# Optimization experiments

Hardware: AMD Instinct MI355X
Metric: run time of the kernel (lower is better)

Reference implementation:

```python
import jax, jax.numpy as jnp
import numpy as np

B, S, H, I, E, K = 2, 512, 512, 1024, 64, 4


def setup_inputs() -> dict:
    key = jax.random.key(0)
    ks = jax.random.split(key, 16)
    scale = jnp.float32(0.02)

    def w(k, shape):
        return jax.random.normal(k, shape, dtype=jnp.float32) * scale

    return {
        "x": jax.random.normal(ks[0], (B, S, H), dtype=jnp.float32),
        "router_w": w(ks[1], (E, H)),
        "router_b": w(ks[2], (E,)),
        "expert_biases": jnp.zeros((E,), dtype=jnp.float32),
        "sw1": w(ks[3], (I, H)), "sb1": w(ks[4], (I,)),
        "sw2": w(ks[5], (H, I)), "sb2": w(ks[6], (H,)),
        "sw3": w(ks[7], (I, H)), "sb3": w(ks[8], (I,)),
        "w1": w(ks[9], (E, I, H)), "b1": w(ks[10], (E, I)),
        "w2": w(ks[11], (E, H, I)), "b2": w(ks[12], (E, H)),
        "w3": w(ks[13], (E, I, H)), "b3": w(ks[14], (E, I)),
        "top_k": K,
    }


def _ffn(x, w1, b1, w2, b2, w3, b3):
    return (jax.nn.silu(x @ w1.T + b1) * (x @ w3.T + b3)) @ w2.T + b2


def reference(x, router_w, router_b, expert_biases,
              sw1, sb1, sw2, sb2, sw3, sb3,
              w1, b1, w2, b2, w3, b3, top_k):
    Bx, Sx, Hx = x.shape
    Ex = router_w.shape[0]

    # Router: logits [B,S,E]; top-k selection uses bias-adjusted logits,
    # but gates come from the ORIGINAL (unbiased) logits.
    logits = x @ router_w.T + router_b
    _, idx = jax.lax.top_k(logits + expert_biases, top_k)  # [B,S,K] int32
    orig = jnp.take_along_axis(logits, idx, axis=-1)       # [B,S,K]
    scores = jax.nn.sigmoid(orig)
    gates = scores / jnp.maximum(jnp.sum(scores, axis=-1, keepdims=True), 1e-12)

    # Shared expert(s): num_shared_experts == 1, divided by 1.
    shared = _ffn(x, sw1, sb1, sw2, sb2, sw3, sb3)

    # Combine gates into a dense per-token per-expert gate matrix [T,E].
    xf = x.reshape(-1, Hx)                 # [T,H]
    T = xf.shape[0]
    tok = jnp.arange(T)[:, None]
    gate_full = jnp.zeros((T, Ex), x.dtype).at[tok, idx.reshape(T, top_k)].add(
        gates.reshape(T, top_k))

    # Routed experts: each expert FFN over all tokens, gated combine.
    # (Mathematically identical to the original masked-dense loop: the mask
    #  zeroes both inputs and gates of unassigned tokens.)
    def body(acc, p):
        ew1, eb1, ew2, eb2, ew3, eb3, g = p
        y = _ffn(xf, ew1, eb1, ew2, eb2, ew3, eb3)  # [T,H]
        return acc + g[:, None] * y, None

    acc, _ = jax.lax.scan(body, jnp.zeros_like(xf),
                          (w1, b1, w2, b2, w3, b3, gate_full.T))

    return shared + acc.reshape(x.shape)
```

## Files before the change

### kernel.cpp

```cpp
#include <hip/hip_runtime.h>
#include <math.h>

#define T_    1024
#define H_    512
#define I_    1024
#define E_    64
#define K_    4
#define NPAIR (T_*K_)
#define NENT  (NPAIR + T_)

#define BM 64
#define BN 64
#define BKS 64
#define LDP 72
#define MAXWORK 160

typedef float  f32x4  __attribute__((ext_vector_type(4)));
typedef short  bf16x8 __attribute__((ext_vector_type(8)));

__device__ __forceinline__ ushort f2bf(float f) {
    uint u = __float_as_uint(f);
    u += 0x7fffu + ((u >> 16) & 1u);
    return (ushort)(u >> 16);
}

__global__ __launch_bounds__(64) void moe_router(
    const float* __restrict__ x, const float* __restrict__ rw,
    const float* __restrict__ rb, const float* __restrict__ eb,
    int* __restrict__ idx_out, float* __restrict__ gate_out)
{
    const int t = blockIdx.x;
    const int lane = threadIdx.x;
    __shared__ float xs[H_];
    __shared__ float lg[E_];
    __shared__ float bs[E_];
    for (int i = lane; i < H_; i += 64) xs[i] = x[(size_t)t*H_ + i];
    bs[lane] = eb[lane];
    __syncthreads();
    float acc = 0.f;
    const float* wrow = rw + (size_t)lane*H_;
    for (int k = 0; k < H_; k += 4) {
        float4 w4 = *reinterpret_cast<const float4*>(wrow + k);
        acc = fmaf(xs[k+0], w4.x, acc);
        acc = fmaf(xs[k+1], w4.y, acc);
        acc = fmaf(xs[k+2], w4.z, acc);
        acc = fmaf(xs[k+3], w4.w, acc);
    }
    lg[lane] = acc + rb[lane];
    __syncthreads();
    if (lane == 0) {
        unsigned long long used = 0ull;
        int sel[K_]; float orig[K_];
        for (int k = 0; k < K_; ++k) {
            float best = -INFINITY; int bi = 0;
            for (int e = 0; e < E_; ++e) {
                if (used & (1ull << e)) continue;
                float v = lg[e] + bs[e];
                if (v > best) { best = v; bi = e; }
            }
            used |= (1ull << bi);
            sel[k] = bi; orig[k] = lg[bi];
        }
        float s[K_]; float sum = 0.f;
        for (int k = 0; k < K_; ++k) { s[k] = 1.f/(1.f + __expf(-orig[k])); sum += s[k]; }
        sum = fmaxf(sum, 1e-12f);
        for (int k = 0; k < K_; ++k) {
            idx_out[t*K_ + k] = sel[k];
            gate_out[t*K_ + k] = s[k] / sum;
        }
    }
}

__global__ __launch_bounds__(256) void moe_build(
    const int* __restrict__ idx, const float* __restrict__ gates,
    int* __restrict__ cnts, int* __restrict__ offs,
    int* __restrict__ entry_token, float* __restrict__ entry_gate,
    int* __restrict__ pair_pos,
    int* __restrict__ blk_e, int* __restrict__ blk_ro, int* __restrict__ nwork)
{
    __shared__ int c[E_];
    __shared__ int run[E_];
    const int tid = threadIdx.x;
    if (tid < E_) c[tid] = 0;
    __syncthreads();
    for (int p = tid; p < NPAIR; p += 256) atomicAdd(&c[idx[p]], 1);
    __syncthreads();
    if (tid == 0) {
        int o = 0;
        for (int e = 0; e < E_; ++e) { run[e] = o; offs[e] = o; cnts[e] = c[e]; o += c[e]; }
        offs[E_] = NPAIR;
        cnts[E_] = T_;
        int nb = 0;
        for (int e = 0; e <= E_; ++e) {
            int n = (e < E_) ? c[e] : T_;
            for (int ro = 0; ro < n; ro += BM) { blk_e[nb] = e; blk_ro[nb] = ro; ++nb; }
        }
        nwork[0] = nb;
    }
    __syncthreads();
    for (int p = tid; p < NPAIR; p += 256) {
        int e = idx[p];
        int pos = atomicAdd(&run[e], 1);
        entry_token[pos] = p / K_;
        entry_gate[pos]  = gates[p];
        pair_pos[p]      = pos;
    }
    for (int t = tid; t < T_; t += 256) {
        entry_token[NPAIR + t] = t;
        entry_gate[NPAIR + t]  = 1.0f;
    }
}

__global__ __launch_bounds__(256) void moe_stage1(
    const float* __restrict__ x,
    const float* __restrict__ w1, const float* __restrict__ b1,
    const float* __restrict__ w3, const float* __restrict__ b3,
    const float* __restrict__ sw1, const float* __restrict__ sb1,
    const float* __restrict__ sw3, const float* __restrict__ sb3,
    const int* __restrict__ cnts, const int* __restrict__ offs,
    const int* __restrict__ entry_token,
    const int* __restrict__ blk_e, const int* __restrict__ blk_ro,
    const int* __restrict__ nwork,
    ushort* __restrict__ h1buf)
{
    const int w = blockIdx.x;
    if (w >= nwork[0]) return;
    const int e  = blk_e[w];
    const int ro = blk_ro[w];
    const int itile = blockIdx.y;
    const int n = cnts[e];
    const int off = offs[e];
    const int rows = min(BM, n - ro);
    const float* W1 = (e < E_) ? (w1 + (size_t)e*I_*H_) : sw1;
    const float* W3 = (e < E_) ? (w3 + (size_t)e*I_*H_) : sw3;
    const float* B1 = (e < E_) ? (b1 + (size_t)e*I_) : sb1;
    const float* B3 = (e < E_) ? (b3 + (size_t)e*I_) : sb3;

    __shared__ ushort Xs [BM][LDP];
    __shared__ ushort W1s[BN][LDP];
    __shared__ ushort W3s[BN][LDP];

    const int tid  = threadIdx.x;
    const int lane = tid & 63;
    const int wid  = tid >> 6;
    const int wm   = wid >> 1;
    const int wn   = wid & 1;
    const int l15  = lane & 15;
    const int lg   = lane >> 4;

    f32x4 acc1[2][2] = {};
    f32x4 acc3[2][2] = {};

    for (int kc = 0; kc < H_; kc += BKS) {
        __syncthreads();
        #pragma unroll
        for (int i = 0; i < 4; ++i) {
            int u = tid + i*256;
            int r = u >> 4, seg = u & 15;
            float4 v = make_float4(0.f,0.f,0.f,0.f);
            if (r < rows) {
                int tok = entry_token[off + ro + r];
                v = *reinterpret_cast<const float4*>(x + (size_t)tok*H_ + kc + seg*4);
            }
            *reinterpret_cast<ushort4*>(&Xs[r][seg*4]) =
                make_ushort4(f2bf(v.x), f2bf(v.y), f2bf(v.z), f2bf(v.w));
        }
        #pragma unroll
        for (int i = 0; i < 4; ++i) {
            int u = tid + i*256;
            int r = u >> 4, seg = u & 15;
            size_t go = (size_t)(itile*BN + r)*H_ + kc + seg*4;
            float4 v1 = *reinterpret_cast<const float4*>(W1 + go);
            float4 v3 = *reinterpret_cast<const float4*>(W3 + go);
            *reinterpret_cast<ushort4*>(&W1s[r][seg*4]) =
                make_ushort4(f2bf(v1.x), f2bf(v1.y), f2bf(v1.z), f2bf(v1.w));
            *reinterpret_cast<ushort4*>(&W3s[r][seg*4]) =
                make_ushort4(f2bf(v3.x), f2bf(v3.y), f2bf(v3.z), f2bf(v3.w));
        }
        __syncthreads();
        #pragma unroll
        for (int s = 0; s < 2; ++s) {
            bf16x8 a[2], bb1[2], bb3[2];
            #pragma unroll
            for (int f = 0; f < 2; ++f) {
                a[f]   = *reinterpret_cast<const bf16x8*>(&Xs [wm*32 + f*16 + l15][s*32 + lg*8]);
                bb1[f] = *reinterpret_cast<const bf16x8*>(&W1s[wn*32 + f*16 + l15][s*32 + lg*8]);
                bb3[f] = *reinterpret_cast<const bf16x8*>(&W3s[wn*32 + f*16 + l15][s*32 + lg*8]);
            }
            #pragma unroll
            for (int fm = 0; fm < 2; ++fm) {
                #pragma unroll
                for (int fn = 0; fn < 2; ++fn) {
                    acc1[fm][fn] = __builtin_amdgcn_mfma_f32_16x16x32_bf16(a[fm], bb1[fn], acc1[fm][fn], 0, 0, 0);
                    acc3[fm][fn] = __builtin_amdgcn_mfma_f32_16x16x32_bf16(a[fm], bb3[fn], acc3[fm][fn], 0, 0, 0);
                }
            }
        }
    }
    #pragma unroll
    for (int fm = 0; fm < 2; ++fm) {
        #pragma unroll
        for (int fn = 0; fn < 2; ++fn) {
            const int col = itile*BN + wn*32 + fn*16 + l15;
            const float bv1 = B1[col];
            const float bv3 = B3[col];
            #pragma unroll
            for (int j = 0; j < 4; ++j) {
                const int rl = wm*32 + fm*16 + lg*4 + j;
                if (rl < rows) {
                    float z1 = acc1[fm][fn][j] + bv1;
                    float z3 = acc3[fm][fn][j] + bv3;
                    float h = z1 / (1.f + __expf(-z1)) * z3;
                    h1buf[(size_t)(off+ro+rl)*I_ + col] = f2bf(h);
                }
            }
        }
    }
}

__global__ __launch_bounds__(256) void moe_stage2(
    const ushort* __restrict__ h1buf,
    const float* __restrict__ w2, const float* __restrict__ b2,
    const float* __restrict__ sw2, const float* __restrict__ sb2,
    const int* __restrict__ cnts, const int* __restrict__ offs,
    const float* __restrict__ entry_gate,
    const int* __restrict__ blk_e, const int* __restrict__ blk_ro,
    const int* __restrict__ nwork,
    float* __restrict__ ybuf)
{
    const int w = blockIdx.x;
    if (w >= nwork[0]) return;
    const int e  = blk_e[w];
    const int ro = blk_ro[w];
    const int htile = blockIdx.y;
    const int n = cnts[e];
    const int off = offs[e];
    const int rows = min(BM, n - ro);
    const float* W2 = (e < E_) ? (w2 + (size_t)e*H_*I_) : sw2;
    const float* B2 = (e < E_) ? (b2 + (size_t)e*H_) : sb2;

    __shared__ ushort Hs[BM][LDP];
    __shared__ ushort Ws[BN][LDP];

    const int tid  = threadIdx.x;
    const int lane = tid & 63;
    const int wid  = tid >> 6;
    const int wm   = wid >> 1;
    const int wn   = wid & 1;
    const int l15  = lane & 15;
    const int lg   = lane >> 4;

    f32x4 acc[2][2] = {};

    for (int kc = 0; kc < I_; kc += BKS) {
        __syncthreads();
        #pragma unroll
        for (int i = 0; i < 2; ++i) {
            int u = tid + i*256;
            int r = u >> 3, seg = u & 7;
            uint4 v = make_uint4(0u,0u,0u,0u);
            if (r < rows)
                v = *reinterpret_cast<const uint4*>(h1buf + (size_t)(off+ro+r)*I_ + kc + seg*8);
            *reinterpret_cast<uint4*>(&Hs[r][seg*8]) = v;
        }
        #pragma unroll
        for (int i = 0; i < 4; ++i) {
            int u = tid + i*256;
            int r = u >> 4, seg = u & 15;
            size_t go = (size_t)(htile*BN + r)*I_ + kc + seg*4;
            float4 v = *reinterpret_cast<const float4*>(W2 + go);
            *reinterpret_cast<ushort4*>(&Ws[r][seg*4]) =
                make_ushort4(f2bf(v.x), f2bf(v.y), f2bf(v.z), f2bf(v.w));
        }
        __syncthreads();
        #pragma unroll
        for (int s = 0; s < 2; ++s) {
            bf16x8 a[2], b[2];
            #pragma unroll
            for (int f = 0; f < 2; ++f) {
                a[f] = *reinterpret_cast<const bf16x8*>(&Hs[wm*32 + f*16 + l15][s*32 + lg*8]);
                b[f] = *reinterpret_cast<const bf16x8*>(&Ws[wn*32 + f*16 + l15][s*32 + lg*8]);
            }
            #pragma unroll
            for (int fm = 0; fm < 2; ++fm) {
                #pragma unroll
                for (int fn = 0; fn < 2; ++fn) {
                    acc[fm][fn] = __builtin_amdgcn_mfma_f32_16x16x32_bf16(a[fm], b[fn], acc[fm][fn], 0, 0, 0);
                }
            }
        }
    }
    #pragma unroll
    for (int fm = 0; fm < 2; ++fm) {
        #pragma unroll
        for (int fn = 0; fn < 2; ++fn) {
            const int col = htile*BN + wn*32 + fn*16 + l15;
            const float bv = B2[col];
            #pragma unroll
            for (int j = 0; j < 4; ++j) {
                const int rl = wm*32 + fm*16 + lg*4 + j;
                if (rl < rows) {
                    const float g = entry_gate[off + ro + rl];
                    ybuf[(size_t)(off+ro+rl)*H_ + col] = (acc[fm][fn][j] + bv) * g;
                }
            }
        }
    }
}

__global__ __launch_bounds__(128) void moe_combine(
    const float* __restrict__ ybuf, const int* __restrict__ pair_pos,
    float* __restrict__ out)
{
    const int t = blockIdx.x;
    const int lane = threadIdx.x;
    const int h = lane * 4;
    const int p0 = pair_pos[t*K_+0], p1 = pair_pos[t*K_+1];
    const int p2 = pair_pos[t*K_+2], p3 = pair_pos[t*K_+3];
    float4 a  = *reinterpret_cast<const float4*>(ybuf + (size_t)(NPAIR+t)*H_ + h);
    float4 v0 = *reinterpret_cast<const float4*>(ybuf + (size_t)p0*H_ + h);
    float4 v1 = *reinterpret_cast<const float4*>(ybuf + (size_t)p1*H_ + h);
    float4 v2 = *reinterpret_cast<const float4*>(ybuf + (size_t)p2*H_ + h);
    float4 v3 = *reinterpret_cast<const float4*>(ybuf + (size_t)p3*H_ + h);
    float4 r;
    r.x = a.x + v0.x + v1.x + v2.x + v3.x;
    r.y = a.y + v0.y + v1.y + v2.y + v3.y;
    r.z = a.z + v0.z + v1.z + v2.z + v3.z;
    r.w = a.w + v0.w + v1.w + v2.w + v3.w;
    *reinterpret_cast<float4*>(out + (size_t)t*H_ + h) = r;
}

extern "C" void kernel_launch(void* const* d_in, const int* in_sizes, int n_in,
                              void* d_out, int out_size, void* d_ws, size_t ws_size,
                              hipStream_t stream)
{
    const float* x   = (const float*)d_in[0];
    const float* rw  = (const float*)d_in[1];
    const float* rb  = (const float*)d_in[2];
    const float* eb  = (const float*)d_in[3];
    const float* sw1 = (const float*)d_in[4];
    const float* sb1 = (const float*)d_in[5];
    const float* sw2 = (const float*)d_in[6];
    const float* sb2 = (const float*)d_in[7];
    const float* sw3 = (const float*)d_in[8];
    const float* sb3 = (const float*)d_in[9];
    const float* w1  = (const float*)d_in[10];
    const float* b1  = (const float*)d_in[11];
    const float* w2  = (const float*)d_in[12];
    const float* b2  = (const float*)d_in[13];
    const float* w3  = (const float*)d_in[14];
    const float* b3  = (const float*)d_in[15];
    float* out = (float*)d_out;

    char* p = (char*)d_ws;
    auto take = [&](size_t bytes) { char* q = p; p += (bytes + 255) & ~(size_t)255; return q; };
    int*    idxb  = (int*)   take((size_t)NPAIR*4);
    float*  gateb = (float*) take((size_t)NPAIR*4);
    int*    cnts  = (int*)   take((E_+1)*4);
    int*    offs  = (int*)   take((E_+1)*4);
    int*    etok  = (int*)   take((size_t)NENT*4);
    float*  egate = (float*) take((size_t)NENT*4);
    int*    ppos  = (int*)   take((size_t)NPAIR*4);
    int*    blk_e = (int*)   take((size_t)MAXWORK*4);
    int*    blk_ro= (int*)   take((size_t)MAXWORK*4);
    int*    nwork = (int*)   take(4);
    ushort* h1buf = (ushort*)take((size_t)NENT*I_*2);
    float*  ybuf  = (float*) take((size_t)NENT*H_*4);

    moe_router <<<T_, 64, 0, stream>>>(x, rw, rb, eb, idxb, gateb);
    moe_build  <<<1, 256, 0, stream>>>(idxb, gateb, cnts, offs, etok, egate, ppos,
                                       blk_e, blk_ro, nwork);
    moe_stage1 <<<dim3(MAXWORK, I_/BN), 256, 0, stream>>>(x, w1, b1, w3, b3,
                                                          sw1, sb1, sw3, sb3,
                                                          cnts, offs, etok,
                                                          blk_e, blk_ro, nwork, h1buf);
    moe_stage2 <<<dim3(MAXWORK, H_/BN), 256, 0, stream>>>(h1buf, w2, b2, sw2, sb2,
                                                          cnts, offs, egate,
                                                          blk_e, blk_ro, nwork, ybuf);
    moe_combine<<<T_, 128, 0, stream>>>(ybuf, ppos, out);
}
```

Baseline: 221.8 us.

## Prefetch next K-chunk into registers to overlap global loads with MFMA

Both grouped GEMM kernels now load the next K-slice of activations and weights into registers before the compute on the current slice. At the top of each iteration those registers are converted to bf16 and written to shared memory. This hides global load latency behind the MFMA work. Row pointers are precomputed once, and the bounds check on partial tiles is dropped, so padding rows now read arbitrary in-range or past-end data instead of zeros.

```diff
diff --git a/kernel.cpp b/kernel.cpp
--- a/kernel.cpp
+++ b/kernel.cpp
@@ -148,34 +148,47 @@
     const int l15  = lane & 15;
     const int lg   = lane >> 4;
 
+    const int sr = tid >> 4;
+    const int sc = tid & 15;
+
+    const float* xp[4];
+    const float* wp[4];
+    #pragma unroll
+    for (int i = 0; i < 4; ++i) {
+        int r = sr + i*16;
+        xp[i] = x + (size_t)entry_token[off + ro + r]*H_ + sc*4;
+        wp[i] = W1 + (size_t)(itile*BN + r)*H_ + sc*4;
+    }
+    const ptrdiff_t d31 = (const float*)W3 - (const float*)W1;
+
     f32x4 acc1[2][2] = {};
     f32x4 acc3[2][2] = {};
 
+    float4 xv[4], av[4], cv[4];
+    #pragma unroll
+    for (int i = 0; i < 4; ++i) {
+        xv[i] = *reinterpret_cast<const float4*>(xp[i]);
+        av[i] = *reinterpret_cast<const float4*>(wp[i]);
+        cv[i] = *reinterpret_cast<const float4*>(wp[i] + d31);
+    }
+
     for (int kc = 0; kc < H_; kc += BKS) {
+        const int kc2 = (kc + BKS) & (H_ - 1);
         __syncthreads();
         #pragma unroll
         for (int i = 0; i < 4; ++i) {
-            int u = tid + i*256;
-            int r = u >> 4, seg = u & 15;
-            float4 v = make_float4(0.f,0.f,0.f,0.f);
-            if (r < rows) {
-                int tok = entry_token[off + ro + r];
-                v = *reinterpret_cast<const float4*>(x + (size_t)tok*H_ + kc + seg*4);
-            }
-            *reinterpret_cast<ushort4*>(&Xs[r][seg*4]) =
-                make_ushort4(f2bf(v.x), f2bf(v.y), f2bf(v.z), f2bf(v.w));
+            *reinterpret_cast<ushort4*>(&Xs [sr + i*16][sc*4]) =
+                make_ushort4(f2bf(xv[i].x), f2bf(xv[i].y), f2bf(xv[i].z), f2bf(xv[i].w));
+            *reinterpret_cast<ushort4*>(&W1s[sr + i*16][sc*4]) =
+                make_ushort4(f2bf(av[i].x), f2bf(av[i].y), f2bf(av[i].z), f2bf(av[i].w));
+            *reinterpret_cast<ushort4*>(&W3s[sr + i*16][sc*4]) =
+                make_ushort4(f2bf(cv[i].x), f2bf(cv[i].y), f2bf(cv[i].z), f2bf(cv[i].w));
         }
         #pragma unroll
         for (int i = 0; i < 4; ++i) {
-            int u = tid + i*256;
-            int r = u >> 4, seg = u & 15;
-            size_t go = (size_t)(itile*BN + r)*H_ + kc + seg*4;
-            float4 v1 = *reinterpret_cast<const float4*>(W1 + go);
-            float4 v3 = *reinterpret_cast<const float4*>(W3 + go);
-            *reinterpret_cast<ushort4*>(&W1s[r][seg*4]) =
-                make_ushort4(f2bf(v1.x), f2bf(v1.y), f2bf(v1.z), f2bf(v1.w));
-            *reinterpret_cast<ushort4*>(&W3s[r][seg*4]) =
-                make_ushort4(f2bf(v3.x), f2bf(v3.y), f2bf(v3.z), f2bf(v3.w));
+            xv[i] = *reinterpret_cast<const float4*>(xp[i] + kc2);
+            av[i] = *reinterpret_cast<const float4*>(wp[i] + kc2);
+            cv[i] = *reinterpret_cast<const float4*>(wp[i] + kc2 + d31);
         }
         __syncthreads();
         #pragma unroll
@@ -250,28 +263,45 @@
     const int l15  = lane & 15;
     const int lg   = lane >> 4;
 
+    const int sr = tid >> 4;
+    const int sc = tid & 15;
+    const int hr = tid >> 3;
+    const int hc = tid & 7;
+
+    const ushort* hp[2];
+    const float*  wp[4];
+    #pragma unroll
+    for (int i = 0; i < 2; ++i)
+        hp[i] = h1buf + (size_t)(off + ro + hr + i*32)*I_ + hc*8;
+    #pragma unroll
+    for (int i = 0; i < 4; ++i)
+        wp[i] = W2 + (size_t)(htile*BN + sr + i*16)*I_ + sc*4;
+
     f32x4 acc[2][2] = {};
 
+    uint4  hv[2];
+    float4 wv[4];
+    #pragma unroll
+    for (int i = 0; i < 2; ++i) hv[i] = *reinterpret_cast<const uint4*>(hp[i]);
+    #pragma unroll
+    for (int i = 0; i < 4; ++i) wv[i] = *reinterpret_cast<const float4*>(wp[i]);
+
     for (int kc = 0; kc < I_; kc += BKS) {
+        const int kc2 = (kc + BKS) & (I_ - 1);
         __syncthreads();
         #pragma unroll
-        for (int i = 0; i < 2; ++i) {
-            int u = tid + i*256;
-            int r = u >> 3, seg = u & 7;
-            uint4 v = make_uint4(0u,0u,0u,0u);
-            if (r < rows)
-                v = *reinterpret_cast<const uint4*>(h1buf + (size_t)(off+ro+r)*I_ + kc + seg*8);
-            *reinterpret_cast<uint4*>(&Hs[r][seg*8]) = v;
-        }
-        #pragma unroll
-        for (int i = 0; i < 4; ++i) {
-            int u = tid + i*256;
-            int r = u >> 4, seg = u & 15;
-            size_t go = (size_t)(htile*BN + r)*I_ + kc + seg*4;
-            float4 v = *reinterpret_cast<const float4*>(W2 + go);
-            *reinterpret_cast<ushort4*>(&Ws[r][seg*4]) =
-                make_ushort4(f2bf(v.x), f2bf(v.y), f2bf(v.z), f2bf(v.w));
-        }
+        for (int i = 0; i < 2; ++i)
+            *reinterpret_cast<uint4*>(&Hs[hr + i*32][hc*8]) = hv[i];
+        #pragma unroll
+        for (int i = 0; i < 4; ++i)
+            *reinterpret_cast<ushort4*>(&Ws[sr + i*16][sc*4]) =
+                make_ushort4(f2bf(wv[i].x), f2bf(wv[i].y), f2bf(wv[i].z), f2bf(wv[i].w));
+        #pragma unroll
+        for (int i = 0; i < 2; ++i)
+            hv[i] = *reinterpret_cast<const uint4*>(hp[i] + kc2);
+        #pragma unroll
+        for (int i = 0; i < 4; ++i)
+            wv[i] = *reinterpret_cast<const float4*>(wp[i] + kc2);
         __syncthreads();
         #pragma unroll
         for (int s = 0; s < 2; ++s) {
```

Result: no change. 221.8 us (-0.0%).

## Double-buffer expert GEMM tiles via async global-to-LDS loads with swizzled layout

Applied to the files above, without the earlier changes.

Both expert GEMM stages now use double-buffered LDS filled with global_load_lds 16-byte async copies, so the next K-tile loads while MFMAs run on the current one. The LDS layout is XOR-swizzled to avoid bank conflicts, and weights stay fp32 in LDS, converted to bf16 as fragments are read. Tokens are pre-converted to bf16 by a new x_cvt kernel, the row tile grows from 64 to 128, and blocks use 512 threads. The trade-offs are a much larger LDS footprint per block, which limits occupancy, repeated fp32-to-bf16 conversion work in the inner loop, and unmasked gathers for rows past the end of a tile.

```diff
diff --git a/kernel.cpp b/kernel.cpp
--- a/kernel.cpp
+++ b/kernel.cpp
@@ -9,10 +9,9 @@
 #define NPAIR (T_*K_)
 #define NENT  (NPAIR + T_)
 
-#define BM 64
+#define BM 128
 #define BN 64
 #define BKS 64
-#define LDP 72
 #define MAXWORK 160
 
 typedef float  f32x4  __attribute__((ext_vector_type(4)));
@@ -22,6 +21,30 @@
     uint u = __float_as_uint(f);
     u += 0x7fffu + ((u >> 16) & 1u);
     return (ushort)(u >> 16);
+}
+
+__device__ __forceinline__ bf16x8 cvt8(f32x4 a, f32x4 b) {
+    bf16x8 r;
+    r[0] = (short)f2bf(a[0]); r[1] = (short)f2bf(a[1]);
+    r[2] = (short)f2bf(a[2]); r[3] = (short)f2bf(a[3]);
+    r[4] = (short)f2bf(b[0]); r[5] = (short)f2bf(b[1]);
+    r[6] = (short)f2bf(b[2]); r[7] = (short)f2bf(b[3]);
+    return r;
+}
+
+__device__ __forceinline__ void gload16(const void* g, void* lds) {
+    __builtin_amdgcn_global_load_lds(
+        (const __attribute__((address_space(1))) unsigned int*)g,
+        (__attribute__((address_space(3))) unsigned int*)lds, 16, 0, 0);
+}
+
+__global__ __launch_bounds__(256) void x_cvt(const float* __restrict__ x,
+                                             ushort* __restrict__ xb)
+{
+    const int i = blockIdx.x*256 + threadIdx.x;
+    float4 v = reinterpret_cast<const float4*>(x)[i];
+    reinterpret_cast<ushort4*>(xb)[i] =
+        make_ushort4(f2bf(v.x), f2bf(v.y), f2bf(v.z), f2bf(v.w));
 }
 
 __global__ __launch_bounds__(64) void moe_router(
@@ -111,8 +134,8 @@
     }
 }
 
-__global__ __launch_bounds__(256) void moe_stage1(
-    const float* __restrict__ x,
+__global__ __launch_bounds__(512, 2) void moe_stage1(
+    const ushort* __restrict__ xbf,
     const float* __restrict__ w1, const float* __restrict__ b1,
     const float* __restrict__ w3, const float* __restrict__ b3,
     const float* __restrict__ sw1, const float* __restrict__ sb1,
@@ -136,9 +159,8 @@
     const float* B1 = (e < E_) ? (b1 + (size_t)e*I_) : sb1;
     const float* B3 = (e < E_) ? (b3 + (size_t)e*I_) : sb3;
 
-    __shared__ ushort Xs [BM][LDP];
-    __shared__ ushort W1s[BN][LDP];
-    __shared__ ushort W3s[BN][LDP];
+    __shared__ ushort XL[2][BM*BKS];
+    __shared__ float  WL[2][2*BN*BKS];
 
     const int tid  = threadIdx.x;
     const int lane = tid & 63;
@@ -148,44 +170,67 @@
     const int l15  = lane & 15;
     const int lg   = lane >> 4;
 
+    const ushort* xsrc[2];
+    #pragma unroll
+    for (int i = 0; i < 2; ++i) {
+        const int j = wid*2 + i;
+        const int r = j*8 + (lane >> 3);
+        const int tok = entry_token[off + ro + r];
+        const int csw = ((lane & 7) ^ (r & 7)) << 3;
+        xsrc[i] = xbf + (size_t)tok*H_ + csw;
+    }
+    const float* wsrc[4];
+    #pragma unroll
+    for (int i = 0; i < 4; ++i) {
+        const int j = wid*4 + i;
+        const int rb = j*4 + (lane >> 4);
+        const float* base = (rb < BN) ? (W1 + (size_t)(itile*BN + rb)*H_)
+                                      : (W3 + (size_t)(itile*BN + rb - BN)*H_);
+        const int c16 = lane & 15;
+        const int csw = ((((c16 >> 1) ^ (rb & 7)) << 3) + ((c16 & 1) << 2));
+        wsrc[i] = base + csw;
+    }
+
     f32x4 acc1[2][2] = {};
     f32x4 acc3[2][2] = {};
 
-    for (int kc = 0; kc < H_; kc += BKS) {
-        __syncthreads();
-        #pragma unroll
-        for (int i = 0; i < 4; ++i) {
-            int u = tid + i*256;
-            int r = u >> 4, seg = u & 15;
-            float4 v = make_float4(0.f,0.f,0.f,0.f);
-            if (r < rows) {
-                int tok = entry_token[off + ro + r];
-                v = *reinterpret_cast<const float4*>(x + (size_t)tok*H_ + kc + seg*4);
-            }
-            *reinterpret_cast<ushort4*>(&Xs[r][seg*4]) =
-                make_ushort4(f2bf(v.x), f2bf(v.y), f2bf(v.z), f2bf(v.w));
-        }
-        #pragma unroll
-        for (int i = 0; i < 4; ++i) {
-            int u = tid + i*256;
-            int r = u >> 4, seg = u & 15;
-            size_t go = (size_t)(itile*BN + r)*H_ + kc + seg*4;
-            float4 v1 = *reinterpret_cast<const float4*>(W1 + go);
-            float4 v3 = *reinterpret_cast<const float4*>(W3 + go);
-            *reinterpret_cast<ushort4*>(&W1s[r][seg*4]) =
-                make_ushort4(f2bf(v1.x), f2bf(v1.y), f2bf(v1.z), f2bf(v1.w));
-            *reinterpret_cast<ushort4*>(&W3s[r][seg*4]) =
-                make_ushort4(f2bf(v3.x), f2bf(v3.y), f2bf(v3.z), f2bf(v3.w));
-        }
-        __syncthreads();
+    #define STAGE1(t, buf)                                                       \
+        do {                                                                     \
+            const int kc_ = (t) * BKS;                                           \
+            _Pragma("unroll")                                                    \
+            for (int i_ = 0; i_ < 2; ++i_)                                       \
+                gload16(xsrc[i_] + kc_, (char*)&XL[buf][0] + (wid*2 + i_)*1024); \
+            _Pragma("unroll")                                                    \
+            for (int i_ = 0; i_ < 4; ++i_)                                       \
+                gload16(wsrc[i_] + kc_, (char*)&WL[buf][0] + (wid*4 + i_)*1024); \
+        } while (0)
+
+    STAGE1(0, 0);
+    __syncthreads();
+
+    const int NT = H_ / BKS;
+    for (int t = 0; t < NT; ++t) {
+        const int cur = t & 1;
+        if (t + 1 < NT) STAGE1(t + 1, cur ^ 1);
+        asm volatile("" ::: "memory");
         #pragma unroll
         for (int s = 0; s < 2; ++s) {
             bf16x8 a[2], bb1[2], bb3[2];
             #pragma unroll
             for (int f = 0; f < 2; ++f) {
-                a[f]   = *reinterpret_cast<const bf16x8*>(&Xs [wm*32 + f*16 + l15][s*32 + lg*8]);
-                bb1[f] = *reinterpret_cast<const bf16x8*>(&W1s[wn*32 + f*16 + l15][s*32 + lg*8]);
-                bb3[f] = *reinterpret_cast<const bf16x8*>(&W3s[wn*32 + f*16 + l15][s*32 + lg*8]);
+                const int rr = wm*32 + f*16 + l15;
+                a[f] = *reinterpret_cast<const bf16x8*>(
+                    (const char*)&XL[cur][0] + rr*128 + ((((s<<2)|lg) ^ (rr&7)) << 4));
+                const int rw = wn*32 + f*16 + l15;
+                const char* p1 = (const char*)&WL[cur][0] + rw*256
+                               + ((((s<<2)|lg) ^ (rw&7)) << 5);
+                f32x4 u0 = *reinterpret_cast<const f32x4*>(p1);
+                f32x4 u1 = *reinterpret_cast<const f32x4*>(p1 + 16);
+                bb1[f] = cvt8(u0, u1);
+                const char* p3 = p1 + BN*256;
+                f32x4 v0 = *reinterpret_cast<const f32x4*>(p3);
+                f32x4 v1 = *reinterpret_cast<const f32x4*>(p3 + 16);
+                bb3[f] = cvt8(v0, v1);
             }
             #pragma unroll
             for (int fm = 0; fm < 2; ++fm) {
@@ -196,7 +241,10 @@
                 }
             }
         }
-    }
+        __syncthreads();
+    }
+    #undef STAGE1
+
     #pragma unroll
     for (int fm = 0; fm < 2; ++fm) {
         #pragma unroll
@@ -218,7 +266,7 @@
     }
 }
 
-__global__ __launch_bounds__(256) void moe_stage2(
+__global__ __launch_bounds__(512, 4) void moe_stage2(
     const ushort* __restrict__ h1buf,
     const float* __restrict__ w2, const float* __restrict__ b2,
     const float* __restrict__ sw2, const float* __restrict__ sb2,
@@ -239,8 +287,8 @@
     const float* W2 = (e < E_) ? (w2 + (size_t)e*H_*I_) : sw2;
     const float* B2 = (e < E_) ? (b2 + (size_t)e*H_) : sb2;
 
-    __shared__ ushort Hs[BM][LDP];
-    __shared__ ushort Ws[BN][LDP];
+    __shared__ ushort HL[2][BM*BKS];
+    __shared__ float  W2L[2][BN*BKS];
 
     const int tid  = threadIdx.x;
     const int lane = tid & 63;
@@ -250,36 +298,59 @@
     const int l15  = lane & 15;
     const int lg   = lane >> 4;
 
+    const ushort* hsrc[2];
+    #pragma unroll
+    for (int i = 0; i < 2; ++i) {
+        const int j = wid*2 + i;
+        const int r = j*8 + (lane >> 3);
+        const int csw = ((lane & 7) ^ (r & 7)) << 3;
+        hsrc[i] = h1buf + (size_t)(off + ro + r)*I_ + csw;
+    }
+    const float* w2src[2];
+    #pragma unroll
+    for (int i = 0; i < 2; ++i) {
+        const int j = wid*2 + i;
+        const int rb = j*4 + (lane >> 4);
+        const int c16 = lane & 15;
+        const int csw = ((((c16 >> 1) ^ (rb & 7)) << 3) + ((c16 & 1) << 2));
+        w2src[i] = W2 + (size_t)(htile*BN + rb)*I_ + csw;
+    }
+
     f32x4 acc[2][2] = {};
 
-    for (int kc = 0; kc < I_; kc += BKS) {
-        __syncthreads();
-        #pragma unroll
-        for (int i = 0; i < 2; ++i) {
-            int u = tid + i*256;
-            int r = u >> 3, seg = u & 7;
-            uint4 v = make_uint4(0u,0u,0u,0u);
-            if (r < rows)
-                v = *reinterpret_cast<const uint4*>(h1buf + (size_t)(off+ro+r)*I_ + kc + seg*8);
-            *reinterpret_cast<uint4*>(&Hs[r][seg*8]) = v;
-        }
-        #pragma unroll
-        for (int i = 0; i < 4; ++i) {
-            int u = tid + i*256;
-            int r = u >> 4, seg = u & 15;
-            size_t go = (size_t)(htile*BN + r)*I_ + kc + seg*4;
-            float4 v = *reinterpret_cast<const float4*>(W2 + go);
-            *reinterpret_cast<ushort4*>(&Ws[r][seg*4]) =
-                make_ushort4(f2bf(v.x), f2bf(v.y), f2bf(v.z), f2bf(v.w));
-        }
-        __syncthreads();
+    #define STAGE2(t, buf)                                                        \
+        do {                                                                      \
+            const int kc_ = (t) * BKS;                                            \
+            _Pragma("unroll")                                                     \
+            for (int i_ = 0; i_ < 2; ++i_)                                        \
+                gload16(hsrc[i_] + kc_, (char*)&HL[buf][0] + (wid*2 + i_)*1024);  \
+            _Pragma("unroll")                                                     \
+            for (int i_ = 0; i_ < 2; ++i_)                                        \
+                gload16(w2src[i_] + kc_, (char*)&W2L[buf][0] + (wid*2 + i_)*1024);\
+        } while (0)
+
+    STAGE2(0, 0);
+    __syncthreads();
+
+    const int NT = I_ / BKS;
+    for (int t = 0; t < NT; ++t) {
+        const int cur = t & 1;
+        if (t + 1 < NT) STAGE2(t + 1, cur ^ 1);
+        asm volatile("" ::: "memory");
         #pragma unroll
         for (int s = 0; s < 2; ++s) {
             bf16x8 a[2], b[2];
             #pragma unroll
             for (int f = 0; f < 2; ++f) {
-                a[f] = *reinterpret_cast<const bf16x8*>(&Hs[wm*32 + f*16 + l15][s*32 + lg*8]);
-                b[f] = *reinterpret_cast<const bf16x8*>(&Ws[wn*32 + f*16 + l15][s*32 + lg*8]);
+                const int rr = wm*32 + f*16 + l15;
+                a[f] = *reinterpret_cast<const bf16x8*>(
+                    (const char*)&HL[cur][0] + rr*128 + ((((s<<2)|lg) ^ (rr&7)) << 4));
+                const int rw = wn*32 + f*16 + l15;
+                const char* p = (const char*)&W2L[cur][0] + rw*256
+                              + ((((s<<2)|lg) ^ (rw&7)) << 5);
+                f32x4 u0 = *reinterpret_cast<const f32x4*>(p);
+                f32x4 u1 = *reinterpret_cast<const f32x4*>(p + 16);
+                b[f] = cvt8(u0, u1);
             }
             #pragma unroll
             for (int fm = 0; fm < 2; ++fm) {
@@ -289,7 +360,10 @@
                 }
             }
         }
-    }
+        __syncthreads();
+    }
+    #undef STAGE2
+
     #pragma unroll
     for (int fm = 0; fm < 2; ++fm) {
         #pragma unroll
@@ -364,17 +438,19 @@
     int*    blk_e = (int*)   take((size_t)MAXWORK*4);
     int*    blk_ro= (int*)   take((size_t)MAXWORK*4);
     int*    nwork = (int*)   take(4);
+    ushort* xbf   = (ushort*)take((size_t)T_*H_*2);
     ushort* h1buf = (ushort*)take((size_t)NENT*I_*2);
     float*  ybuf  = (float*) take((size_t)NENT*H_*4);
 
+    x_cvt      <<<(T_*H_)/(256*4), 256, 0, stream>>>(x, xbf);
     moe_router <<<T_, 64, 0, stream>>>(x, rw, rb, eb, idxb, gateb);
     moe_build  <<<1, 256, 0, stream>>>(idxb, gateb, cnts, offs, etok, egate, ppos,
                                        blk_e, blk_ro, nwork);
-    moe_stage1 <<<dim3(MAXWORK, I_/BN), 256, 0, stream>>>(x, w1, b1, w3, b3,
+    moe_stage1 <<<dim3(MAXWORK, I_/BN), 512, 0, stream>>>(xbf, w1, b1, w3, b3,
                                                           sw1, sb1, sw3, sb3,
                                                           cnts, offs, etok,
                                                           blk_e, blk_ro, nwork, h1buf);
-    moe_stage2 <<<dim3(MAXWORK, H_/BN), 256, 0, stream>>>(h1buf, w2, b2, sw2, sb2,
+    moe_stage2 <<<dim3(MAXWORK, H_/BN), 512, 0, stream>>>(h1buf, w2, b2, sw2, sb2,
                                                           cnts, offs, egate,
                                                           blk_e, blk_ro, nwork, ybuf);
     moe_combine<<<T_, 128, 0, stream>>>(ybuf, ppos, out);
```

Result: slower. 244.3 us (+10.2%).

## Use direct global-to-LDS swizzled loads, 128-row tiles and pre-converted bf16 activations

Applied to the files above, without the earlier changes.

Both expert GEMM stages now stage tiles with global_load_lds 16-byte transfers into XOR-swizzled shared memory instead of register round-trips with padded arrays. Weights stay fp32 in shared memory and are converted to bf16 while fragments are read. The row tile grows from 64 to 128 so each expert's weights are streamed fewer times when it has more than 64 tokens. Activations are converted to bf16 once by a new kernel, and occupancy hints are added. Tail rows beyond a group's count are now loaded from neighbouring entries rather than zero-filled, and loads are not double-buffered.

```diff
diff --git a/kernel.cpp b/kernel.cpp
--- a/kernel.cpp
+++ b/kernel.cpp
@@ -9,11 +9,12 @@
 #define NPAIR (T_*K_)
 #define NENT  (NPAIR + T_)
 
-#define BM 64
+#define BM 128
 #define BN 64
 #define BKS 64
-#define LDP 72
 #define MAXWORK 160
+#define NT1 (H_/BKS)
+#define NT2 (I_/BKS)
 
 typedef float  f32x4  __attribute__((ext_vector_type(4)));
 typedef short  bf16x8 __attribute__((ext_vector_type(8)));
@@ -22,6 +23,29 @@
     uint u = __float_as_uint(f);
     u += 0x7fffu + ((u >> 16) & 1u);
     return (ushort)(u >> 16);
+}
+__device__ __forceinline__ bf16x8 cvt8(f32x4 a, f32x4 b) {
+    bf16x8 r;
+    r[0] = (short)f2bf(a[0]); r[1] = (short)f2bf(a[1]);
+    r[2] = (short)f2bf(a[2]); r[3] = (short)f2bf(a[3]);
+    r[4] = (short)f2bf(b[0]); r[5] = (short)f2bf(b[1]);
+    r[6] = (short)f2bf(b[2]); r[7] = (short)f2bf(b[3]);
+    return r;
+}
+
+__device__ __forceinline__ void gload16(const void* g, void* lds) {
+    __builtin_amdgcn_global_load_lds(
+        (const __attribute__((address_space(1))) unsigned int*)g,
+        (__attribute__((address_space(3))) unsigned int*)lds, 16, 0, 0);
+}
+
+__global__ __launch_bounds__(256) void x_cvt(const float* __restrict__ x,
+                                             ushort* __restrict__ xb)
+{
+    const int i = blockIdx.x*256 + threadIdx.x;
+    float4 v = reinterpret_cast<const float4*>(x)[i];
+    reinterpret_cast<ushort4*>(xb)[i] =
+        make_ushort4(f2bf(v.x), f2bf(v.y), f2bf(v.z), f2bf(v.w));
 }
 
 __global__ __launch_bounds__(64) void moe_router(
@@ -111,8 +135,8 @@
     }
 }
 
-__global__ __launch_bounds__(256) void moe_stage1(
-    const float* __restrict__ x,
+__global__ __launch_bounds__(256, 3) void moe_stage1(
+    const ushort* __restrict__ xbf,
     const float* __restrict__ w1, const float* __restrict__ b1,
     const float* __restrict__ w3, const float* __restrict__ b3,
     const float* __restrict__ sw1, const float* __restrict__ sb1,
@@ -136,9 +160,9 @@
     const float* B1 = (e < E_) ? (b1 + (size_t)e*I_) : sb1;
     const float* B3 = (e < E_) ? (b3 + (size_t)e*I_) : sb3;
 
-    __shared__ ushort Xs [BM][LDP];
-    __shared__ ushort W1s[BN][LDP];
-    __shared__ ushort W3s[BN][LDP];
+    __shared__ __align__(16) ushort XL [BM*BKS];
+    __shared__ __align__(16) float  W1L[BN*BKS];
+    __shared__ __align__(16) float  W3L[BN*BKS];
 
     const int tid  = threadIdx.x;
     const int lane = tid & 63;
@@ -148,57 +172,72 @@
     const int l15  = lane & 15;
     const int lg   = lane >> 4;
 
-    f32x4 acc1[2][2] = {};
-    f32x4 acc3[2][2] = {};
-
-    for (int kc = 0; kc < H_; kc += BKS) {
+    const ushort* xsrc[4];
+    const float* w1src[4];
+    const float* w3src[4];
+    #pragma unroll
+    for (int i = 0; i < 4; ++i) {
+        const int j = wid*4 + i;
+        const int rX = j*8 + (lane >> 3);
+        const int cX = (lane & 7) ^ (rX & 7);
+        xsrc[i] = xbf + (size_t)entry_token[off + ro + rX]*H_ + cX*8;
+        const int rW = j*4 + (lane >> 4);
+        const int c32 = ((lane & 15) >> 1) ^ (rW & 7);
+        const int colW = c32*8 + (lane & 1)*4;
+        w1src[i] = W1 + (size_t)(itile*BN + rW)*H_ + colW;
+        w3src[i] = W3 + (size_t)(itile*BN + rW)*H_ + colW;
+    }
+
+    f32x4 acc1[4][2] = {};
+    f32x4 acc3[4][2] = {};
+
+    for (int t = 0; t < NT1; ++t) {
+        const int kc = t * BKS;
+        #pragma unroll
+        for (int i = 0; i < 4; ++i)
+            gload16(xsrc[i] + kc, (char*)XL + (wid*4 + i)*1024);
+        #pragma unroll
+        for (int i = 0; i < 4; ++i)
+            gload16(w1src[i] + kc, (char*)W1L + (wid*4 + i)*1024);
+        #pragma unroll
+        for (int i = 0; i < 4; ++i)
+            gload16(w3src[i] + kc, (char*)W3L + (wid*4 + i)*1024);
         __syncthreads();
         #pragma unroll
-        for (int i = 0; i < 4; ++i) {
-            int u = tid + i*256;
-            int r = u >> 4, seg = u & 15;
-            float4 v = make_float4(0.f,0.f,0.f,0.f);
-            if (r < rows) {
-                int tok = entry_token[off + ro + r];
-                v = *reinterpret_cast<const float4*>(x + (size_t)tok*H_ + kc + seg*4);
-            }
-            *reinterpret_cast<ushort4*>(&Xs[r][seg*4]) =
-                make_ushort4(f2bf(v.x), f2bf(v.y), f2bf(v.z), f2bf(v.w));
-        }
-        #pragma unroll
-        for (int i = 0; i < 4; ++i) {
-            int u = tid + i*256;
-            int r = u >> 4, seg = u & 15;
-            size_t go = (size_t)(itile*BN + r)*H_ + kc + seg*4;
-            float4 v1 = *reinterpret_cast<const float4*>(W1 + go);
-            float4 v3 = *reinterpret_cast<const float4*>(W3 + go);
-            *reinterpret_cast<ushort4*>(&W1s[r][seg*4]) =
-                make_ushort4(f2bf(v1.x), f2bf(v1.y), f2bf(v1.z), f2bf(v1.w));
-            *reinterpret_cast<ushort4*>(&W3s[r][seg*4]) =
-                make_ushort4(f2bf(v3.x), f2bf(v3.y), f2bf(v3.z), f2bf(v3.w));
-        }
-        __syncthreads();
-        #pragma unroll
         for (int s = 0; s < 2; ++s) {
-            bf16x8 a[2], bb1[2], bb3[2];
-            #pragma unroll
-            for (int f = 0; f < 2; ++f) {
-                a[f]   = *reinterpret_cast<const bf16x8*>(&Xs [wm*32 + f*16 + l15][s*32 + lg*8]);
-                bb1[f] = *reinterpret_cast<const bf16x8*>(&W1s[wn*32 + f*16 + l15][s*32 + lg*8]);
-                bb3[f] = *reinterpret_cast<const bf16x8*>(&W3s[wn*32 + f*16 + l15][s*32 + lg*8]);
-            }
-            #pragma unroll
-            for (int fm = 0; fm < 2; ++fm) {
+            bf16x8 a[4];
+            #pragma unroll
+            for (int fm = 0; fm < 4; ++fm) {
+                const int rr = wm*64 + fm*16 + l15;
+                a[fm] = *reinterpret_cast<const bf16x8*>(
+                    (const char*)XL + rr*128 + (((s*4 + lg) ^ (rr & 7)) << 4));
+            }
+            bf16x8 b1f[2], b3f[2];
+            #pragma unroll
+            for (int fn = 0; fn < 2; ++fn) {
+                const int rw = wn*32 + fn*16 + l15;
+                const int cw = ((s*4 + lg) ^ (rw & 7)) << 5;
+                const char* p1 = (const char*)W1L + rw*256 + cw;
+                b1f[fn] = cvt8(*reinterpret_cast<const f32x4*>(p1),
+                               *reinterpret_cast<const f32x4*>(p1 + 16));
+                const char* p3 = (const char*)W3L + rw*256 + cw;
+                b3f[fn] = cvt8(*reinterpret_cast<const f32x4*>(p3),
+                               *reinterpret_cast<const f32x4*>(p3 + 16));
+            }
+            #pragma unroll
+            for (int fm = 0; fm < 4; ++fm) {
                 #pragma unroll
                 for (int fn = 0; fn < 2; ++fn) {
-                    acc1[fm][fn] = __builtin_amdgcn_mfma_f32_16x16x32_bf16(a[fm], bb1[fn], acc1[fm][fn], 0, 0, 0);
-                    acc3[fm][fn] = __builtin_amdgcn_mfma_f32_16x16x32_bf16(a[fm], bb3[fn], acc3[fm][fn], 0, 0, 0);
+                    acc1[fm][fn] = __builtin_amdgcn_mfma_f32_16x16x32_bf16(a[fm], b1f[fn], acc1[fm][fn], 0, 0, 0);
+                    acc3[fm][fn] = __builtin_amdgcn_mfma_f32_16x16x32_bf16(a[fm], b3f[fn], acc3[fm][fn], 0, 0, 0);
                 }
             }
         }
-    }
+        __syncthreads();
+    }
+
     #pragma unroll
-    for (int fm = 0; fm < 2; ++fm) {
+    for (int fm = 0; fm < 4; ++fm) {
         #pragma unroll
         for (int fn = 0; fn < 2; ++fn) {
             const int col = itile*BN + wn*32 + fn*16 + l15;
@@ -206,7 +245,7 @@
             const float bv3 = B3[col];
             #pragma unroll
             for (int j = 0; j < 4; ++j) {
-                const int rl = wm*32 + fm*16 + lg*4 + j;
+                const int rl = wm*64 + fm*16 + lg*4 + j;
                 if (rl < rows) {
                     float z1 = acc1[fm][fn][j] + bv1;
                     float z3 = acc3[fm][fn][j] + bv3;
@@ -218,7 +257,7 @@
     }
 }
 
-__global__ __launch_bounds__(256) void moe_stage2(
+__global__ __launch_bounds__(256, 4) void moe_stage2(
     const ushort* __restrict__ h1buf,
     const float* __restrict__ w2, const float* __restrict__ b2,
     const float* __restrict__ sw2, const float* __restrict__ sb2,
@@ -239,8 +278,8 @@
     const float* W2 = (e < E_) ? (w2 + (size_t)e*H_*I_) : sw2;
     const float* B2 = (e < E_) ? (b2 + (size_t)e*H_) : sb2;
 
-    __shared__ ushort Hs[BM][LDP];
-    __shared__ ushort Ws[BN][LDP];
+    __shared__ __align__(16) ushort HL [BM*BKS];
+    __shared__ __align__(16) float  W2L[BN*BKS];
 
     const int tid  = threadIdx.x;
     const int lane = tid & 63;
@@ -250,55 +289,67 @@
     const int l15  = lane & 15;
     const int lg   = lane >> 4;
 
-    f32x4 acc[2][2] = {};
-
-    for (int kc = 0; kc < I_; kc += BKS) {
+    const ushort* hsrc[4];
+    const float*  wsrc[4];
+    #pragma unroll
+    for (int i = 0; i < 4; ++i) {
+        const int j = wid*4 + i;
+        const int rH = j*8 + (lane >> 3);
+        const int cH = (lane & 7) ^ (rH & 7);
+        hsrc[i] = h1buf + (size_t)(off + ro + rH)*I_ + cH*8;
+        const int rW = j*4 + (lane >> 4);
+        const int c32 = ((lane & 15) >> 1) ^ (rW & 7);
+        wsrc[i] = W2 + (size_t)(htile*BN + rW)*I_ + c32*8 + (lane & 1)*4;
+    }
+
+    f32x4 acc[4][2] = {};
+
+    for (int t = 0; t < NT2; ++t) {
+        const int kc = t * BKS;
+        #pragma unroll
+        for (int i = 0; i < 4; ++i)
+            gload16(hsrc[i] + kc, (char*)HL + (wid*4 + i)*1024);
+        #pragma unroll
+        for (int i = 0; i < 4; ++i)
+            gload16(wsrc[i] + kc, (char*)W2L + (wid*4 + i)*1024);
         __syncthreads();
         #pragma unroll
-        for (int i = 0; i < 2; ++i) {
-            int u = tid + i*256;
-            int r = u >> 3, seg = u & 7;
-            uint4 v = make_uint4(0u,0u,0u,0u);
-            if (r < rows)
-                v = *reinterpret_cast<const uint4*>(h1buf + (size_t)(off+ro+r)*I_ + kc + seg*8);
-            *reinterpret_cast<uint4*>(&Hs[r][seg*8]) = v;
-        }
-        #pragma unroll
-        for (int i = 0; i < 4; ++i) {
-            int u = tid + i*256;
-            int r = u >> 4, seg = u & 15;
-            size_t go = (size_t)(htile*BN + r)*I_ + kc + seg*4;
-            float4 v = *reinterpret_cast<const float4*>(W2 + go);
-            *reinterpret_cast<ushort4*>(&Ws[r][seg*4]) =
-                make_ushort4(f2bf(v.x), f2bf(v.y), f2bf(v.z), f2bf(v.w));
-        }
-        __syncthreads();
-        #pragma unroll
         for (int s = 0; s < 2; ++s) {
-            bf16x8 a[2], b[2];
-            #pragma unroll
-            for (int f = 0; f < 2; ++f) {
-                a[f] = *reinterpret_cast<const bf16x8*>(&Hs[wm*32 + f*16 + l15][s*32 + lg*8]);
-                b[f] = *reinterpret_cast<const bf16x8*>(&Ws[wn*32 + f*16 + l15][s*32 + lg*8]);
-            }
-            #pragma unroll
-            for (int fm = 0; fm < 2; ++fm) {
+            bf16x8 a[4];
+            #pragma unroll
+            for (int fm = 0; fm < 4; ++fm) {
+                const int rr = wm*64 + fm*16 + l15;
+                a[fm] = *reinterpret_cast<const bf16x8*>(
+                    (const char*)HL + rr*128 + (((s*4 + lg) ^ (rr & 7)) << 4));
+            }
+            bf16x8 bf[2];
+            #pragma unroll
+            for (int fn = 0; fn < 2; ++fn) {
+                const int rw = wn*32 + fn*16 + l15;
+                const char* p = (const char*)W2L + rw*256 + (((s*4 + lg) ^ (rw & 7)) << 5);
+                bf[fn] = cvt8(*reinterpret_cast<const f32x4*>(p),
+                              *reinterpret_cast<const f32x4*>(p + 16));
+            }
+            #pragma unroll
+            for (int fm = 0; fm < 4; ++fm) {
                 #pragma unroll
                 for (int fn = 0; fn < 2; ++fn) {
-                    acc[fm][fn] = __builtin_amdgcn_mfma_f32_16x16x32_bf16(a[fm], b[fn], acc[fm][fn], 0, 0, 0);
+                    acc[fm][fn] = __builtin_amdgcn_mfma_f32_16x16x32_bf16(a[fm], bf[fn], acc[fm][fn], 0, 0, 0);
                 }
             }
         }
-    }
+        __syncthreads();
+    }
+
     #pragma unroll
-    for (int fm = 0; fm < 2; ++fm) {
+    for (int fm = 0; fm < 4; ++fm) {
         #pragma unroll
         for (int fn = 0; fn < 2; ++fn) {
             const int col = htile*BN + wn*32 + fn*16 + l15;
             const float bv = B2[col];
             #pragma unroll
             for (int j = 0; j < 4; ++j) {
-                const int rl = wm*32 + fm*16 + lg*4 + j;
+                const int rl = wm*64 + fm*16 + lg*4 + j;
                 if (rl < rows) {
                     const float g = entry_gate[off + ro + rl];
                     ybuf[(size_t)(off+ro+rl)*H_ + col] = (acc[fm][fn][j] + bv) * g;
@@ -364,13 +415,15 @@
     int*    blk_e = (int*)   take((size_t)MAXWORK*4);
     int*    blk_ro= (int*)   take((size_t)MAXWORK*4);
     int*    nwork = (int*)   take(4);
+    ushort* xbf   = (ushort*)take((size_t)T_*H_*2);
     ushort* h1buf = (ushort*)take((size_t)NENT*I_*2);
     float*  ybuf  = (float*) take((size_t)NENT*H_*4);
 
+    x_cvt      <<<(T_*H_)/(256*4), 256, 0, stream>>>(x, xbf);
     moe_router <<<T_, 64, 0, stream>>>(x, rw, rb, eb, idxb, gateb);
     moe_build  <<<1, 256, 0, stream>>>(idxb, gateb, cnts, offs, etok, egate, ppos,
                                        blk_e, blk_ro, nwork);
-    moe_stage1 <<<dim3(MAXWORK, I_/BN), 256, 0, stream>>>(x, w1, b1, w3, b3,
+    moe_stage1 <<<dim3(MAXWORK, I_/BN), 256, 0, stream>>>(xbf, w1, b1, w3, b3,
                                                           sw1, sb1, sw3, sb3,
                                                           cnts, offs, etok,
                                                           blk_e, blk_ro, nwork, h1buf);
```

Result: faster. 201.7 us (-9.1%).
